# Kernel optimization log

Hardware: AMD Instinct MI355X
Metric: run time of the kernel (lower is better)

## Reference

```python
import jax, jax.numpy as jnp
import numpy as np

B, N, K = 8, 2048, 20
EMB = 1024


def _knn(x, k):
    # x: (B, C, N) -> indices of k nearest neighbors (B, N, k) by negative sq. distance
    xx = jnp.sum(x * x, axis=1)                      # (B, N)
    inner = jnp.einsum('bcn,bcm->bnm', x, x)         # (B, N, N)
    neg_d = 2.0 * inner - xx[:, :, None] - xx[:, None, :]
    return jax.lax.top_k(neg_d, k)[1]


def _graph_feature(x, idx):
    # x: (B, C, N), idx: (B, N, k) -> (B, 2C, N, k) = concat(neighbor - center, center)
    nb = jnp.take_along_axis(x[:, :, None, :], idx[:, None, :, :], axis=3)  # (B,C,N,k)
    xc = x[:, :, :, None]
    return jnp.concatenate([nb - xc, jnp.broadcast_to(xc, nb.shape)], axis=1)


def _cbl2(e, W, s, b):
    # 1x1 Conv2d (no bias) + BatchNorm(eval, folded to affine) + LeakyReLU(0.2)
    y = jnp.einsum('oc,bcnk->bonk', W, e)
    return jax.nn.leaky_relu(y * s[None, :, None, None] + b[None, :, None, None], 0.2)


def _cbl1(x, W, s, b):
    y = jnp.einsum('oc,bcn->bon', W, x)
    return jax.nn.leaky_relu(y * s[None, :, None] + b[None, :, None], 0.2)


def setup_inputs() -> dict:
    key = jax.random.key(0)
    ks = jax.random.split(key, 64)
    i = [0]

    def nk():
        i[0] += 1
        return ks[i[0]]

    def w(o, c):
        return jax.random.normal(nk(), (o, c), jnp.float32) * np.float32(1.0 / np.sqrt(c))

    def sb(c):
        s = jax.random.uniform(nk(), (c,), jnp.float32, 0.5, 1.5)
        b = jax.random.normal(nk(), (c,), jnp.float32) * 0.1
        return s, b

    inp = {'x': jax.random.normal(nk(), (B, 9, N), jnp.float32)}
    inp['w1a'] = w(64, 18);  inp['s1a'], inp['b1a'] = sb(64)
    inp['w1b'] = w(64, 64);  inp['s1b'], inp['b1b'] = sb(64)
    inp['w2a'] = w(64, 128); inp['s2a'], inp['b2a'] = sb(64)
    inp['w2b'] = w(64, 64);  inp['s2b'], inp['b2b'] = sb(64)
    inp['w3'] = w(64, 128);  inp['s3'], inp['b3'] = sb(64)
    inp['w4'] = w(EMB, 192); inp['s4'], inp['b4'] = sb(EMB)
    inp['w5a'] = w(512, EMB + 192); inp['s5a'], inp['b5a'] = sb(512)
    inp['w5b'] = w(256, 512); inp['s5b'], inp['b5b'] = sb(256)
    inp['w6'] = w(13, 256)
    return inp


def reference(x, w1a, s1a, b1a, w1b, s1b, b1b, w2a, s2a, b2a, w2b, s2b, b2b,
              w3, s3, b3, w4, s4, b4, w5a, s5a, b5a, w5b, s5b, b5b, w6):
    # EdgeConv block 1 (knn on xyz channels 6:9)
    e = _graph_feature(x, _knn(x[:, 6:], K))          # (B, 18, N, K)
    e = _cbl2(_cbl2(e, w1a, s1a, b1a), w1b, s1b, b1b)
    x1 = e.max(axis=-1)                               # (B, 64, N)
    # EdgeConv block 2
    e = _graph_feature(x1, _knn(x1, K))               # (B, 128, N, K)
    e = _cbl2(_cbl2(e, w2a, s2a, b2a), w2b, s2b, b2b)
    x2 = e.max(axis=-1)
    # EdgeConv block 3
    e = _graph_feature(x2, _knn(x2, K))
    e = _cbl2(e, w3, s3, b3)
    x3 = e.max(axis=-1)

    xc = jnp.concatenate([x1, x2, x3], axis=1)        # (B, 192, N)
    x4 = _cbl1(xc, w4, s4, b4)                        # (B, EMB, N)
    g = jnp.broadcast_to(x4.max(axis=-1, keepdims=True), (B, EMB, N))
    h = jnp.concatenate([g, x1, x2, x3], axis=1)      # (B, EMB+192, N)
    h = _cbl1(_cbl1(h, w5a, s5a, b5a), w5b, s5b, b5b)
    # dropout in eval mode == identity
    return jnp.einsum('oc,bcn->bon', w6, h)           # (B, 13, N)
```

## Files before the change

### kernel.cpp

```cpp
#include <hip/hip_runtime.h>
#include <cstddef>
#include <cstdint>

namespace {

constexpr int NBATCH = 8;
constexpr int NPTS = 2048;
constexpr int KNN = 20;

__device__ __forceinline__ float lrelu(float v) { return fmaxf(v, 0.2f * v); }

template <int C>
__global__ __launch_bounds__(256) void knn_kernel(const float* __restrict__ x, int chStride,
                                                  int bStride, int* __restrict__ idxOut) {
  constexpr int CP = (C + 3) & ~3;
  constexpr int MT = 128;
  constexpr int ROWS = 32;
  constexpr int RPW = 8;
  constexpr int DS = MT + 4;
  constexpr int NT = NPTS / MT;

  __shared__ float qt[ROWS * CP];
  __shared__ float xt[CP * MT];
  __shared__ float dist[ROWS * DS];

  const int tid = threadIdx.x;
  const int lane = tid & 63;
  const int wv = tid >> 6;
  const int r0 = wv * RPW;
  const int b = blockIdx.x / (NPTS / ROWS);
  const int n0 = (blockIdx.x % (NPTS / ROWS)) * ROWS;
  const float* xb = x + (size_t)b * bStride;

  for (int t = tid; t < ROWS * CP; t += 256) {
    int r = t / CP, c = t % CP;
    qt[r * CP + c] = (c < C) ? xb[(size_t)c * chStride + n0 + r] : 0.f;
  }
  __syncthreads();

  float xn[RPW];
#pragma unroll
  for (int r = 0; r < RPW; ++r) {
    float s = 0.f;
#pragma unroll
    for (int cb = 0; cb < CP; cb += 4) {
      float4 qv = *(const float4*)&qt[(r0 + r) * CP + cb];
      s = fmaf(qv.x, qv.x, s);
      s = fmaf(qv.y, qv.y, s);
      s = fmaf(qv.z, qv.z, s);
      s = fmaf(qv.w, qv.w, s);
    }
    xn[r] = s;
  }

  const int srow = tid >> 3;
  const int ssub = tid & 7;
  double lv[KNN];
#pragma unroll
  for (int s = 0; s < KNN; ++s) lv[s] = -1.0;

#pragma unroll 1
  for (int mt = 0; mt < NT; ++mt) {
    __syncthreads();
    {
      const float4 z4 = make_float4(0.f, 0.f, 0.f, 0.f);
      for (int t = tid; t < CP * MT / 4; t += 256) {
        int f = t * 4;
        int c = f >> 7, m = f & (MT - 1);
        *(float4*)&xt[f] =
            (c < C) ? *(const float4*)&xb[(size_t)c * chStride + mt * MT + m] : z4;
      }
    }
    __syncthreads();

    float acc0[RPW], acc1[RPW];
    float xm0 = 0.f, xm1 = 0.f;
#pragma unroll
    for (int r = 0; r < RPW; ++r) { acc0[r] = 0.f; acc1[r] = 0.f; }
#pragma unroll 1
    for (int cb = 0; cb < CP; cb += 4) {
      float x00 = xt[(cb + 0) * MT + lane];
      float x01 = xt[(cb + 1) * MT + lane];
      float x02 = xt[(cb + 2) * MT + lane];
      float x03 = xt[(cb + 3) * MT + lane];
      float x10 = xt[(cb + 0) * MT + 64 + lane];
      float x11 = xt[(cb + 1) * MT + 64 + lane];
      float x12 = xt[(cb + 2) * MT + 64 + lane];
      float x13 = xt[(cb + 3) * MT + 64 + lane];
      xm0 = fmaf(x00, x00, xm0);
      xm0 = fmaf(x01, x01, xm0);
      xm0 = fmaf(x02, x02, xm0);
      xm0 = fmaf(x03, x03, xm0);
      xm1 = fmaf(x10, x10, xm1);
      xm1 = fmaf(x11, x11, xm1);
      xm1 = fmaf(x12, x12, xm1);
      xm1 = fmaf(x13, x13, xm1);
#pragma unroll
      for (int r = 0; r < RPW; ++r) {
        float4 qv = *(const float4*)&qt[(r0 + r) * CP + cb];
        acc0[r] = fmaf(qv.x, x00, acc0[r]);
        acc0[r] = fmaf(qv.y, x01, acc0[r]);
        acc0[r] = fmaf(qv.z, x02, acc0[r]);
        acc0[r] = fmaf(qv.w, x03, acc0[r]);
        acc1[r] = fmaf(qv.x, x10, acc1[r]);
        acc1[r] = fmaf(qv.y, x11, acc1[r]);
        acc1[r] = fmaf(qv.z, x12, acc1[r]);
        acc1[r] = fmaf(qv.w, x13, acc1[r]);
      }
    }
#pragma unroll
    for (int r = 0; r < RPW; ++r) {
      dist[(r0 + r) * DS + lane] = 2.f * acc0[r] - xn[r] - xm0;
      dist[(r0 + r) * DS + 64 + lane] = 2.f * acc1[r] - xn[r] - xm1;
    }

#pragma unroll 4
    for (int j = 0; j < MT / 8; ++j) {
      float val = dist[srow * DS + j * 8 + ssub];
      int gidx = mt * MT + j * 8 + ssub;
      unsigned int u = __float_as_uint(val);
      u ^= (unsigned int)(((int)u) >> 31) | 0x80000000u;
      unsigned long long key =
          ((unsigned long long)u << 30) | ((unsigned long long)(2047 - gidx) << 19);
      double kd = __longlong_as_double((long long)key);
#pragma unroll
      for (int s = 0; s < KNN - 1; ++s) lv[s] = fmin(lv[s + 1], fmax(lv[s], kd));
      lv[KNN - 1] = fmax(lv[KNN - 1], kd);
    }
  }

  int* op = idxOut + ((size_t)b * NPTS + n0 + srow) * KNN;
#pragma unroll 1
  for (int round = 0; round < KNN; ++round) {
    double bv = lv[KNN - 1];
    bv = fmax(bv, __shfl_xor(bv, 1));
    bv = fmax(bv, __shfl_xor(bv, 2));
    bv = fmax(bv, __shfl_xor(bv, 4));
    if (lv[KNN - 1] == bv) {
#pragma unroll
      for (int s = KNN - 1; s > 0; --s) lv[s] = lv[s - 1];
      lv[0] = -1.0;
    }
    if (ssub == 0)
      op[round] =
          2047 - (int)((unsigned long long)(__double_as_longlong(bv) >> 19) & 0x7FFull);
  }
}

template <int C>
__global__ __launch_bounds__(256) __attribute__((amdgpu_waves_per_eu(4, 4))) void
pointconv_kernel(const float* __restrict__ x, int bStride, const float* __restrict__ W,
                 float* __restrict__ znb, float* __restrict__ base) {
  const int blk = blockIdx.x;
  const int b = blk >> 5;
  const int nc = blk & 31;
  const int nl = threadIdx.x & 63;
  const int q = __builtin_amdgcn_readfirstlane(threadIdx.x >> 6);
  const int n = nc * 64 + nl;
  const float* xb = x + (size_t)b * bStride;

  float fz[16], fb[16];
#pragma unroll
  for (int t = 0; t < 16; ++t) { fz[t] = 0.f; fb[t] = 0.f; }
#pragma unroll 4
  for (int c = 0; c < C; ++c) {
    float xv = xb[(size_t)c * NPTS + n];
#pragma unroll
    for (int t = 0; t < 16; ++t) {
      float w0 = W[(q * 16 + t) * 2 * C + c];
      float w1 = W[(q * 16 + t) * 2 * C + C + c];
      fz[t] = fmaf(w0, xv, fz[t]);
      fb[t] = fmaf(w1 - w0, xv, fb[t]);
    }
  }
  const size_t o0 = ((size_t)(b * NPTS + n)) * 64 + q * 16;
#pragma unroll
  for (int t = 0; t < 16; t += 4)
    *(float4*)&znb[o0 + t] = make_float4(fz[t], fz[t + 1], fz[t + 2], fz[t + 3]);
#pragma unroll
  for (int t = 0; t < 16; t += 4)
    *(float4*)&base[o0 + t] = make_float4(fb[t], fb[t + 1], fb[t + 2], fb[t + 3]);
}

template <bool TWO>
__global__ __launch_bounds__(256) __attribute__((amdgpu_waves_per_eu(2, 4))) void edge_kernel(
    const float* __restrict__ znb, const float* __restrict__ base,
    const int* __restrict__ idx, const float* __restrict__ s1, const float* __restrict__ b1,
    const float* __restrict__ W2, const float* __restrict__ s2, const float* __restrict__ b2,
    float* __restrict__ xout) {
  __shared__ float baseS[12][64];
  const int tid = threadIdx.x;
  const int gp0 = blockIdx.x * 12;

  for (int t = tid; t < 12 * 64; t += 256) {
    int p = t >> 6, cp = t & 63;
    int gpt = gp0 + p;
    baseS[p][cp] = (gpt < NBATCH * NPTS) ? base[(size_t)gpt * 64 + cp] : 0.f;
  }
  __syncthreads();

  const int lane = tid & 63;
  const int wv = __builtin_amdgcn_readfirstlane(tid >> 6);
  int p = lane / 20;
  const int k = lane - p * 20;
  const bool pact = (p < 3);
  if (!pact) p = 2;
  const int pl = wv * 3 + p;
  const int gpt = gp0 + pl;
  const bool act = pact && (gpt < NBATCH * NPTS);
  const int gptc = (gpt < NBATCH * NPTS) ? gpt : (NBATCH * NPTS - 1);
  const int bb = gptc >> 11;
  const int nn = gptc & (NPTS - 1);
  const int m = idx[(size_t)gptc * KNN + k];
  const float* zg = znb + ((size_t)bb * NPTS + m) * 64;

  float y1[64];
#pragma unroll
  for (int c4 = 0; c4 < 64; c4 += 4) {
    float4 zv = *(const float4*)&zg[c4];
    float4 bv = *(const float4*)&baseS[pl][c4];
    y1[c4 + 0] = zv.x + bv.x;
    y1[c4 + 1] = zv.y + bv.y;
    y1[c4 + 2] = zv.z + bv.z;
    y1[c4 + 3] = zv.w + bv.w;
  }
#pragma unroll
  for (int cp = 0; cp < 64; ++cp) y1[cp] = lrelu(fmaf(y1[cp], s1[cp], b1[cp]));

  if constexpr (TWO) {
#pragma unroll 2
    for (int o2 = 0; o2 < 64; ++o2) {
      float a = 0.f;
#pragma unroll
      for (int c = 0; c < 64; ++c) a = fmaf(W2[o2 * 64 + c], y1[c], a);
      float z = lrelu(fmaf(a, s2[o2], b2[o2]));
#pragma unroll
      for (int off = 1; off < 32; off <<= 1) {
        float ov = __shfl_down(z, off);
        if (k + off < KNN) z = fmaxf(z, ov);
      }
      if (act && k == 0) xout[((size_t)bb * 64 + o2) * NPTS + nn] = z;
    }
  } else {
#pragma unroll 2
    for (int o2 = 0; o2 < 64; ++o2) {
      float z = y1[o2];
#pragma unroll
      for (int off = 1; off < 32; off <<= 1) {
        float ov = __shfl_down(z, off);
        if (k + off < KNN) z = fmaxf(z, ov);
      }
      if (act && k == 0) xout[((size_t)bb * 64 + o2) * NPTS + nn] = z;
    }
  }
}

__global__ __launch_bounds__(256) void x4max_kernel(const float* __restrict__ x1,
                                                    const float* __restrict__ x2,
                                                    const float* __restrict__ x3,
                                                    const float* __restrict__ W4,
                                                    const float* __restrict__ s4,
                                                    const float* __restrict__ b4,
                                                    float* __restrict__ pmax) {
  const int blk = blockIdx.x;
  const int b = blk >> 10;
  const int oc = (blk >> 5) & 31;
  const int nc = blk & 31;
  const int nl = threadIdx.x & 63;
  const int q = __builtin_amdgcn_readfirstlane(threadIdx.x >> 6);
  const int n = nc * 64 + nl;
  const float* xA = x1 + (size_t)b * 64 * NPTS;
  const float* xB = x2 + (size_t)b * 64 * NPTS;
  const float* xC = x3 + (size_t)b * 64 * NPTS;
  const float* wq = W4 + (size_t)(oc * 32 + q * 8) * 192;

  float f[8];
#pragma unroll
  for (int t = 0; t < 8; ++t) f[t] = 0.f;
#pragma unroll 2
  for (int cb = 0; cb < 64; cb += 4) {
    float xv0 = xA[(size_t)(cb + 0) * NPTS + n];
    float xv1 = xA[(size_t)(cb + 1) * NPTS + n];
    float xv2 = xA[(size_t)(cb + 2) * NPTS + n];
    float xv3 = xA[(size_t)(cb + 3) * NPTS + n];
#pragma unroll
    for (int t = 0; t < 8; ++t) {
      float4 wv = *(const float4*)&wq[(size_t)t * 192 + cb];
      f[t] = fmaf(wv.x, xv0, f[t]);
      f[t] = fmaf(wv.y, xv1, f[t]);
      f[t] = fmaf(wv.z, xv2, f[t]);
      f[t] = fmaf(wv.w, xv3, f[t]);
    }
  }
#pragma unroll 2
  for (int cb = 0; cb < 64; cb += 4) {
    float xv0 = xB[(size_t)(cb + 0) * NPTS + n];
    float xv1 = xB[(size_t)(cb + 1) * NPTS + n];
    float xv2 = xB[(size_t)(cb + 2) * NPTS + n];
    float xv3 = xB[(size_t)(cb + 3) * NPTS + n];
#pragma unroll
    for (int t = 0; t < 8; ++t) {
      float4 wv = *(const float4*)&wq[(size_t)t * 192 + 64 + cb];
      f[t] = fmaf(wv.x, xv0, f[t]);
      f[t] = fmaf(wv.y, xv1, f[t]);
      f[t] = fmaf(wv.z, xv2, f[t]);
      f[t] = fmaf(wv.w, xv3, f[t]);
    }
  }
#pragma unroll 2
  for (int cb = 0; cb < 64; cb += 4) {
    float xv0 = xC[(size_t)(cb + 0) * NPTS + n];
    float xv1 = xC[(size_t)(cb + 1) * NPTS + n];
    float xv2 = xC[(size_t)(cb + 2) * NPTS + n];
    float xv3 = xC[(size_t)(cb + 3) * NPTS + n];
#pragma unroll
    for (int t = 0; t < 8; ++t) {
      float4 wv = *(const float4*)&wq[(size_t)t * 192 + 128 + cb];
      f[t] = fmaf(wv.x, xv0, f[t]);
      f[t] = fmaf(wv.y, xv1, f[t]);
      f[t] = fmaf(wv.z, xv2, f[t]);
      f[t] = fmaf(wv.w, xv3, f[t]);
    }
  }
#pragma unroll
  for (int t = 0; t < 8; ++t) {
    const int o = oc * 32 + q * 8 + t;
    float v = lrelu(fmaf(f[t], s4[o], b4[o]));
#pragma unroll
    for (int off = 32; off; off >>= 1) v = fmaxf(v, __shfl_down(v, off));
    if (nl == 0) pmax[(size_t)(b * 1024 + o) * 32 + nc] = v;
  }
}

__global__ __launch_bounds__(256) void gmax_kernel(const float* __restrict__ pmax,
                                                   float* __restrict__ g) {
  int i = blockIdx.x * 256 + threadIdx.x;
  if (i >= NBATCH * 1024) return;
  float v = -__builtin_inff();
#pragma unroll
  for (int j = 0; j < 32; ++j) v = fmaxf(v, pmax[(size_t)i * 32 + j]);
  g[i] = v;
}

__global__ __launch_bounds__(256) void t5a_kernel(const float* __restrict__ g,
                                                  const float* __restrict__ w5a,
                                                  float* __restrict__ t5a) {
  const int task = blockIdx.x * 4 + (threadIdx.x >> 6);
  const int lane = threadIdx.x & 63;
  const int b = task >> 9;
  const int o5 = task & 511;
  float acc = 0.f;
  for (int c = lane; c < 1024; c += 64) acc = fmaf(w5a[(size_t)o5 * 1216 + c], g[b * 1024 + c], acc);
#pragma unroll
  for (int off = 32; off; off >>= 1) acc += __shfl_down(acc, off);
  if (lane == 0) t5a[task] = acc;
}

__global__ __launch_bounds__(1024) __attribute__((amdgpu_waves_per_eu(4, 4))) void head_kernel(
    const float* __restrict__ x1, const float* __restrict__ x2, const float* __restrict__ x3,
    const float* __restrict__ t5a, const float* __restrict__ w5a, const float* __restrict__ s5a,
    const float* __restrict__ b5a, const float* __restrict__ w5b, const float* __restrict__ s5b,
    const float* __restrict__ b5b, const float* __restrict__ w6, float* __restrict__ out) {
  __shared__ float xls[192 * 64];
  __shared__ float als[2][64 * 64];
  const int tid = threadIdx.x;
  const int nl = tid & 63;
  const int q = __builtin_amdgcn_readfirstlane(tid >> 6);
  const int blk = blockIdx.x;
  const int b = blk >> 5;
  const int n0 = (blk & 31) * 64;

  for (int t = tid; t < 192 * 64; t += 1024) {
    int c = t >> 6, j = t & 63;
    const float* xp = (c < 64) ? x1 : ((c < 128) ? x2 : x3);
    xls[t] = xp[((size_t)b * 64 + (c & 63)) * NPTS + n0 + j];
  }
  __syncthreads();

  float h2[16];
#pragma unroll
  for (int t = 0; t < 16; ++t) h2[t] = 0.f;

#pragma unroll 1
  for (int ch = 0; ch < 8; ++ch) {
    float a[4];
#pragma unroll
    for (int t = 0; t < 4; ++t) a[t] = t5a[b * 512 + ch * 64 + q + 16 * t];
#pragma unroll 4
    for (int cb = 0; cb < 192; cb += 4) {
      float xv0 = xls[(cb + 0) * 64 + nl];
      float xv1 = xls[(cb + 1) * 64 + nl];
      float xv2 = xls[(cb + 2) * 64 + nl];
      float xv3 = xls[(cb + 3) * 64 + nl];
#pragma unroll
      for (int t = 0; t < 4; ++t) {
        float4 wv = *(const float4*)&w5a[(size_t)(ch * 64 + q + 16 * t) * 1216 + 1024 + cb];
        a[t] = fmaf(wv.x, xv0, a[t]);
        a[t] = fmaf(wv.y, xv1, a[t]);
        a[t] = fmaf(wv.z, xv2, a[t]);
        a[t] = fmaf(wv.w, xv3, a[t]);
      }
    }
    float* alsb = als[ch & 1];
#pragma unroll
    for (int t = 0; t < 4; ++t) {
      const int oa = ch * 64 + q + 16 * t;
      alsb[(q + 16 * t) * 64 + nl] = lrelu(fmaf(a[t], s5a[oa], b5a[oa]));
    }
    __syncthreads();
#pragma unroll 2
    for (int ca = 0; ca < 64; ca += 4) {
      float av0 = alsb[(ca + 0) * 64 + nl];
      float av1 = alsb[(ca + 1) * 64 + nl];
      float av2 = alsb[(ca + 2) * 64 + nl];
      float av3 = alsb[(ca + 3) * 64 + nl];
#pragma unroll
      for (int t = 0; t < 16; ++t) {
        float4 wv = *(const float4*)&w5b[(size_t)(q + 16 * t) * 512 + ch * 64 + ca];
        h2[t] = fmaf(wv.x, av0, h2[t]);
        h2[t] = fmaf(wv.y, av1, h2[t]);
        h2[t] = fmaf(wv.z, av2, h2[t]);
        h2[t] = fmaf(wv.w, av3, h2[t]);
      }
    }
  }
#pragma unroll
  for (int t = 0; t < 16; ++t) {
    const int o2 = q + 16 * t;
    h2[t] = lrelu(fmaf(h2[t], s5b[o2], b5b[o2]));
  }
  float pq[13];
#pragma unroll
  for (int o = 0; o < 13; ++o) {
    float s = 0.f;
#pragma unroll
    for (int t = 0; t < 16; ++t) s = fmaf(w6[o * 256 + q + 16 * t], h2[t], s);
    pq[o] = s;
  }
  __syncthreads();
  if (q < 8) {
#pragma unroll
    for (int o = 0; o < 13; ++o) xls[(q * 13 + o) * 64 + nl] = pq[o];
  }
  __syncthreads();
  if (q >= 8) {
#pragma unroll
    for (int o = 0; o < 13; ++o) xls[((q - 8) * 13 + o) * 64 + nl] += pq[o];
  }
  __syncthreads();
  for (int t = tid; t < 13 * 64; t += 1024) {
    int o = t >> 6, j = t & 63;
    float s = 0.f;
#pragma unroll
    for (int qq = 0; qq < 8; ++qq) s += xls[(qq * 13 + o) * 64 + j];
    out[((size_t)b * 13 + o) * NPTS + n0 + j] = s;
  }
}

}

extern "C" void kernel_launch(void* const* d_in, const int* in_sizes, int n_in, void* d_out,
                              int out_size, void* d_ws, size_t ws_size, hipStream_t stream) {
  (void)in_sizes; (void)n_in; (void)out_size;
  const float* x = (const float*)d_in[0];
  const float* w1a = (const float*)d_in[1];
  const float* s1a = (const float*)d_in[2];
  const float* b1a = (const float*)d_in[3];
  const float* w1b = (const float*)d_in[4];
  const float* s1b = (const float*)d_in[5];
  const float* b1b = (const float*)d_in[6];
  const float* w2a = (const float*)d_in[7];
  const float* s2a = (const float*)d_in[8];
  const float* b2a = (const float*)d_in[9];
  const float* w2b = (const float*)d_in[10];
  const float* s2b = (const float*)d_in[11];
  const float* b2b = (const float*)d_in[12];
  const float* w3 = (const float*)d_in[13];
  const float* s3 = (const float*)d_in[14];
  const float* b3 = (const float*)d_in[15];
  const float* w4 = (const float*)d_in[16];
  const float* s4 = (const float*)d_in[17];
  const float* b4 = (const float*)d_in[18];
  const float* w5a = (const float*)d_in[19];
  const float* s5a = (const float*)d_in[20];
  const float* b5a = (const float*)d_in[21];
  const float* w5b = (const float*)d_in[22];
  const float* s5b = (const float*)d_in[23];
  const float* b5b = (const float*)d_in[24];
  const float* w6 = (const float*)d_in[25];
  float* out = (float*)d_out;

  char* wsp = (char*)d_ws;
  size_t off = 0;
  auto alloc = [&](size_t bytes) -> void* {
    void* p = wsp + off;
    off += (bytes + 255) & ~(size_t)255;
    return p;
  };
  int* idx1 = (int*)alloc((size_t)NBATCH * NPTS * KNN * 4);
  int* idx2 = (int*)alloc((size_t)NBATCH * NPTS * KNN * 4);
  int* idx3 = (int*)alloc((size_t)NBATCH * NPTS * KNN * 4);
  float* x1 = (float*)alloc((size_t)NBATCH * 64 * NPTS * 4);
  float* x2 = (float*)alloc((size_t)NBATCH * 64 * NPTS * 4);
  float* x3 = (float*)alloc((size_t)NBATCH * 64 * NPTS * 4);
  float* znbBuf = (float*)alloc((size_t)NBATCH * NPTS * 64 * 4);
  float* baseBuf = (float*)alloc((size_t)NBATCH * NPTS * 64 * 4);
  float* pmaxb = (float*)alloc((size_t)NBATCH * 1024 * 32 * 4);
  float* g = (float*)alloc((size_t)NBATCH * 1024 * 4);
  float* t5a = (float*)alloc((size_t)NBATCH * 512 * 4);

  if (off > ws_size) return;

  const int knnGrid = NBATCH * NPTS / 32;
  const int ecGrid = (NBATCH * NPTS + 11) / 12;
  const int pcGrid = NBATCH * 32;

  knn_kernel<3><<<knnGrid, 256, 0, stream>>>(x + 6 * NPTS, NPTS, 9 * NPTS, idx1);
  pointconv_kernel<9><<<pcGrid, 256, 0, stream>>>(x, 9 * NPTS, w1a, znbBuf, baseBuf);
  edge_kernel<true><<<ecGrid, 256, 0, stream>>>(znbBuf, baseBuf, idx1, s1a, b1a, w1b, s1b, b1b,
                                                x1);
  knn_kernel<64><<<knnGrid, 256, 0, stream>>>(x1, NPTS, 64 * NPTS, idx2);
  pointconv_kernel<64><<<pcGrid, 256, 0, stream>>>(x1, 64 * NPTS, w2a, znbBuf, baseBuf);
  edge_kernel<true><<<ecGrid, 256, 0, stream>>>(znbBuf, baseBuf, idx2, s2a, b2a, w2b, s2b, b2b,
                                                x2);
  knn_kernel<64><<<knnGrid, 256, 0, stream>>>(x2, NPTS, 64 * NPTS, idx3);
  pointconv_kernel<64><<<pcGrid, 256, 0, stream>>>(x2, 64 * NPTS, w3, znbBuf, baseBuf);
  edge_kernel<false><<<ecGrid, 256, 0, stream>>>(znbBuf, baseBuf, idx3, s3, b3, nullptr, nullptr,
                                                 nullptr, x3);
  x4max_kernel<<<8192, 256, 0, stream>>>(x1, x2, x3, w4, s4, b4, pmaxb);
  gmax_kernel<<<32, 256, 0, stream>>>(pmaxb, g);
  t5a_kernel<<<1024, 256, 0, stream>>>(g, w5a, t5a);
  head_kernel<<<256, 1024, 0, stream>>>(x1, x2, x3, t5a, w5a, s5a, b5a, w5b, s5b, b5b, w6, out);
}
```

Before: 1.051 ms.

## Split fused head kernel into three separate layer kernels with global intermediates

Replaces the single fused head kernel (256 blocks of 1024 threads, keeping h1 in LDS and h2 in registers) with three kernels: h1 (conv5a from x1/x2/x3 plus the t5a term), h2 (conv5b) and out (w6 projection). Each writes its intermediate to global workspace (h1 is 8x512x2048, h2 is 8x256x2048). The goal is more blocks and more parallelism, since the fused version ran only 256 blocks and redundantly re-read w5b per point tile. In exchange it adds about 50MB of global writes and reads plus two extra launches, and the out kernel runs only 64 blocks.

```diff
diff --git a/kernel.cpp b/kernel.cpp
--- a/kernel.cpp
+++ b/kernel.cpp
@@ -356,105 +356,143 @@
   if (lane == 0) t5a[task] = acc;
 }
 
-__global__ __launch_bounds__(1024) __attribute__((amdgpu_waves_per_eu(4, 4))) void head_kernel(
-    const float* __restrict__ x1, const float* __restrict__ x2, const float* __restrict__ x3,
-    const float* __restrict__ t5a, const float* __restrict__ w5a, const float* __restrict__ s5a,
-    const float* __restrict__ b5a, const float* __restrict__ w5b, const float* __restrict__ s5b,
-    const float* __restrict__ b5b, const float* __restrict__ w6, float* __restrict__ out) {
-  __shared__ float xls[192 * 64];
-  __shared__ float als[2][64 * 64];
-  const int tid = threadIdx.x;
-  const int nl = tid & 63;
-  const int q = __builtin_amdgcn_readfirstlane(tid >> 6);
+__global__ __launch_bounds__(256) void h1_kernel(const float* __restrict__ x1,
+                                                 const float* __restrict__ x2,
+                                                 const float* __restrict__ x3,
+                                                 const float* __restrict__ t5a,
+                                                 const float* __restrict__ w5a,
+                                                 const float* __restrict__ s5a,
+                                                 const float* __restrict__ b5a,
+                                                 float* __restrict__ h1) {
   const int blk = blockIdx.x;
-  const int b = blk >> 5;
-  const int n0 = (blk & 31) * 64;
-
-  for (int t = tid; t < 192 * 64; t += 1024) {
-    int c = t >> 6, j = t & 63;
-    const float* xp = (c < 64) ? x1 : ((c < 128) ? x2 : x3);
-    xls[t] = xp[((size_t)b * 64 + (c & 63)) * NPTS + n0 + j];
-  }
-  __syncthreads();
-
-  float h2[16];
-#pragma unroll
-  for (int t = 0; t < 16; ++t) h2[t] = 0.f;
-
-#pragma unroll 1
-  for (int ch = 0; ch < 8; ++ch) {
-    float a[4];
-#pragma unroll
-    for (int t = 0; t < 4; ++t) a[t] = t5a[b * 512 + ch * 64 + q + 16 * t];
-#pragma unroll 4
-    for (int cb = 0; cb < 192; cb += 4) {
-      float xv0 = xls[(cb + 0) * 64 + nl];
-      float xv1 = xls[(cb + 1) * 64 + nl];
-      float xv2 = xls[(cb + 2) * 64 + nl];
-      float xv3 = xls[(cb + 3) * 64 + nl];
-#pragma unroll
-      for (int t = 0; t < 4; ++t) {
-        float4 wv = *(const float4*)&w5a[(size_t)(ch * 64 + q + 16 * t) * 1216 + 1024 + cb];
-        a[t] = fmaf(wv.x, xv0, a[t]);
-        a[t] = fmaf(wv.y, xv1, a[t]);
-        a[t] = fmaf(wv.z, xv2, a[t]);
-        a[t] = fmaf(wv.w, xv3, a[t]);
-      }
-    }
-    float* alsb = als[ch & 1];
-#pragma unroll
-    for (int t = 0; t < 4; ++t) {
-      const int oa = ch * 64 + q + 16 * t;
-      alsb[(q + 16 * t) * 64 + nl] = lrelu(fmaf(a[t], s5a[oa], b5a[oa]));
-    }
-    __syncthreads();
-#pragma unroll 2
-    for (int ca = 0; ca < 64; ca += 4) {
-      float av0 = alsb[(ca + 0) * 64 + nl];
-      float av1 = alsb[(ca + 1) * 64 + nl];
-      float av2 = alsb[(ca + 2) * 64 + nl];
-      float av3 = alsb[(ca + 3) * 64 + nl];
-#pragma unroll
-      for (int t = 0; t < 16; ++t) {
-        float4 wv = *(const float4*)&w5b[(size_t)(q + 16 * t) * 512 + ch * 64 + ca];
-        h2[t] = fmaf(wv.x, av0, h2[t]);
-        h2[t] = fmaf(wv.y, av1, h2[t]);
-        h2[t] = fmaf(wv.z, av2, h2[t]);
-        h2[t] = fmaf(wv.w, av3, h2[t]);
-      }
-    }
-  }
-#pragma unroll
-  for (int t = 0; t < 16; ++t) {
-    const int o2 = q + 16 * t;
-    h2[t] = lrelu(fmaf(h2[t], s5b[o2], b5b[o2]));
-  }
-  float pq[13];
-#pragma unroll
-  for (int o = 0; o < 13; ++o) {
-    float s = 0.f;
-#pragma unroll
-    for (int t = 0; t < 16; ++t) s = fmaf(w6[o * 256 + q + 16 * t], h2[t], s);
-    pq[o] = s;
-  }
-  __syncthreads();
-  if (q < 8) {
-#pragma unroll
-    for (int o = 0; o < 13; ++o) xls[(q * 13 + o) * 64 + nl] = pq[o];
-  }
-  __syncthreads();
-  if (q >= 8) {
-#pragma unroll
-    for (int o = 0; o < 13; ++o) xls[((q - 8) * 13 + o) * 64 + nl] += pq[o];
-  }
-  __syncthreads();
-  for (int t = tid; t < 13 * 64; t += 1024) {
-    int o = t >> 6, j = t & 63;
-    float s = 0.f;
-#pragma unroll
-    for (int qq = 0; qq < 8; ++qq) s += xls[(qq * 13 + o) * 64 + j];
-    out[((size_t)b * 13 + o) * NPTS + n0 + j] = s;
-  }
+  const int b = blk >> 9;
+  const int oc = (blk >> 5) & 15;
+  const int nc = blk & 31;
+  const int nl = threadIdx.x & 63;
+  const int q = __builtin_amdgcn_readfirstlane(threadIdx.x >> 6);
+  const int n = nc * 64 + nl;
+  const int o0 = oc * 32 + q * 8;
+  const float* xA = x1 + (size_t)b * 64 * NPTS;
+  const float* xB = x2 + (size_t)b * 64 * NPTS;
+  const float* xC = x3 + (size_t)b * 64 * NPTS;
+  const float* wq = w5a + (size_t)o0 * 1216 + 1024;
+
+  float f[8];
+#pragma unroll
+  for (int t = 0; t < 8; ++t) f[t] = t5a[b * 512 + o0 + t];
+#pragma unroll 2
+  for (int cb = 0; cb < 64; cb += 4) {
+    float xv0 = xA[(size_t)(cb + 0) * NPTS + n];
+    float xv1 = xA[(size_t)(cb + 1) * NPTS + n];
+    float xv2 = xA[(size_t)(cb + 2) * NPTS + n];
+    float xv3 = xA[(size_t)(cb + 3) * NPTS + n];
+#pragma unroll
+    for (int t = 0; t < 8; ++t) {
+      float4 wv = *(const float4*)&wq[(size_t)t * 1216 + cb];
+      f[t] = fmaf(wv.x, xv0, f[t]);
+      f[t] = fmaf(wv.y, xv1, f[t]);
+      f[t] = fmaf(wv.z, xv2, f[t]);
+      f[t] = fmaf(wv.w, xv3, f[t]);
+    }
+  }
+#pragma unroll 2
+  for (int cb = 0; cb < 64; cb += 4) {
+    float xv0 = xB[(size_t)(cb + 0) * NPTS + n];
+    float xv1 = xB[(size_t)(cb + 1) * NPTS + n];
+    float xv2 = xB[(size_t)(cb + 2) * NPTS + n];
+    float xv3 = xB[(size_t)(cb + 3) * NPTS + n];
+#pragma unroll
+    for (int t = 0; t < 8; ++t) {
+      float4 wv = *(const float4*)&wq[(size_t)t * 1216 + 64 + cb];
+      f[t] = fmaf(wv.x, xv0, f[t]);
+      f[t] = fmaf(wv.y, xv1, f[t]);
+      f[t] = fmaf(wv.z, xv2, f[t]);
+      f[t] = fmaf(wv.w, xv3, f[t]);
+    }
+  }
+#pragma unroll 2
+  for (int cb = 0; cb < 64; cb += 4) {
+    float xv0 = xC[(size_t)(cb + 0) * NPTS + n];
+    float xv1 = xC[(size_t)(cb + 1) * NPTS + n];
+    float xv2 = xC[(size_t)(cb + 2) * NPTS + n];
+    float xv3 = xC[(size_t)(cb + 3) * NPTS + n];
+#pragma unroll
+    for (int t = 0; t < 8; ++t) {
+      float4 wv = *(const float4*)&wq[(size_t)t * 1216 + 128 + cb];
+      f[t] = fmaf(wv.x, xv0, f[t]);
+      f[t] = fmaf(wv.y, xv1, f[t]);
+      f[t] = fmaf(wv.z, xv2, f[t]);
+      f[t] = fmaf(wv.w, xv3, f[t]);
+    }
+  }
+#pragma unroll
+  for (int t = 0; t < 8; ++t) {
+    const int o = o0 + t;
+    h1[((size_t)b * 512 + o) * NPTS + n] = lrelu(fmaf(f[t], s5a[o], b5a[o]));
+  }
+}
+
+__global__ __launch_bounds__(256) void h2_kernel(const float* __restrict__ h1,
+                                                 const float* __restrict__ w5b,
+                                                 const float* __restrict__ s5b,
+                                                 const float* __restrict__ b5b,
+                                                 float* __restrict__ h2) {
+  const int blk = blockIdx.x;
+  const int b = blk >> 8;
+  const int oc = (blk >> 5) & 7;
+  const int nc = blk & 31;
+  const int nl = threadIdx.x & 63;
+  const int q = __builtin_amdgcn_readfirstlane(threadIdx.x >> 6);
+  const int n = nc * 64 + nl;
+  const int o0 = oc * 32 + q * 8;
+  const float* hb = h1 + (size_t)b * 512 * NPTS;
+  const float* wq = w5b + (size_t)o0 * 512;
+
+  float f[8];
+#pragma unroll
+  for (int t = 0; t < 8; ++t) f[t] = 0.f;
+#pragma unroll 2
+  for (int cb = 0; cb < 512; cb += 4) {
+    float xv0 = hb[(size_t)(cb + 0) * NPTS + n];
+    float xv1 = hb[(size_t)(cb + 1) * NPTS + n];
+    float xv2 = hb[(size_t)(cb + 2) * NPTS + n];
+    float xv3 = hb[(size_t)(cb + 3) * NPTS + n];
+#pragma unroll
+    for (int t = 0; t < 8; ++t) {
+      float4 wv = *(const float4*)&wq[(size_t)t * 512 + cb];
+      f[t] = fmaf(wv.x, xv0, f[t]);
+      f[t] = fmaf(wv.y, xv1, f[t]);
+      f[t] = fmaf(wv.z, xv2, f[t]);
+      f[t] = fmaf(wv.w, xv3, f[t]);
+    }
+  }
+#pragma unroll
+  for (int t = 0; t < 8; ++t) {
+    const int o = o0 + t;
+    h2[((size_t)b * 256 + o) * NPTS + n] = lrelu(fmaf(f[t], s5b[o], b5b[o]));
+  }
+}
+
+__global__ __launch_bounds__(256) void out_kernel(const float* __restrict__ h2,
+                                                  const float* __restrict__ w6,
+                                                  float* __restrict__ out) {
+  const int blk = blockIdx.x;
+  const int b = blk >> 3;
+  const int nc = blk & 7;
+  const int n = nc * 256 + threadIdx.x;
+  const float* hb = h2 + (size_t)b * 256 * NPTS;
+
+  float f[13];
+#pragma unroll
+  for (int o = 0; o < 13; ++o) f[o] = 0.f;
+#pragma unroll 2
+  for (int c = 0; c < 256; ++c) {
+    float hv = hb[(size_t)c * NPTS + n];
+#pragma unroll
+    for (int o = 0; o < 13; ++o) f[o] = fmaf(w6[o * 256 + c], hv, f[o]);
+  }
+#pragma unroll
+  for (int o = 0; o < 13; ++o) out[((size_t)b * 13 + o) * NPTS + n] = f[o];
 }
 
 }
@@ -508,6 +546,8 @@
   float* pmaxb = (float*)alloc((size_t)NBATCH * 1024 * 32 * 4);
   float* g = (float*)alloc((size_t)NBATCH * 1024 * 4);
   float* t5a = (float*)alloc((size_t)NBATCH * 512 * 4);
+  float* h1 = (float*)alloc((size_t)NBATCH * 512 * NPTS * 4);
+  float* h2 = (float*)alloc((size_t)NBATCH * 256 * NPTS * 4);
 
   if (off > ws_size) return;
 
@@ -530,5 +570,7 @@
   x4max_kernel<<<8192, 256, 0, stream>>>(x1, x2, x3, w4, s4, b4, pmaxb);
   gmax_kernel<<<32, 256, 0, stream>>>(pmaxb, g);
   t5a_kernel<<<1024, 256, 0, stream>>>(g, w5a, t5a);
-  head_kernel<<<256, 1024, 0, stream>>>(x1, x2, x3, t5a, w5a, s5a, b5a, w5b, s5b, b5b, w6, out);
-}
+  h1_kernel<<<4096, 256, 0, stream>>>(x1, x2, x3, t5a, w5a, s5a, b5a, h1);
+  h2_kernel<<<2048, 256, 0, stream>>>(h1, w5b, s5b, b5b, h2);
+  out_kernel<<<64, 256, 0, stream>>>(h2, w6, out);
+}
```

Result: slower. 1.086 ms (+3.3%).
